# Kernel optimization log

Hardware: AMD Instinct MI355X
Metric: run time of the kernel (lower is better)

Reference implementation:

```python
import jax, jax.numpy as jnp
import numpy as np

N = 100000
E = 1600000
IN_DIM, H1, H2, C = 256, 128, 128, 32


def setup_inputs() -> dict:
    key = jax.random.key(0)
    ks = jax.random.split(key, 8)
    X = jax.random.normal(ks[0], (N, IN_DIM), dtype=jnp.float32)
    edge_index = jax.random.randint(ks[1], (2, E), 0, N, dtype=jnp.int64)
    def glorot(k, shape):
        fan_in, fan_out = shape[0], shape[1]
        lim = (6.0 / (fan_in + fan_out)) ** 0.5
        return jax.random.uniform(k, shape, jnp.float32, -lim, lim)
    W1 = glorot(ks[2], (IN_DIM, H1))
    b1 = jnp.zeros((H1,), jnp.float32)
    W2 = glorot(ks[3], (H1, H2))
    b2 = jnp.zeros((H2,), jnp.float32)
    Wc = glorot(ks[4], (H2, C))
    bc = jnp.zeros((C,), jnp.float32)
    return {"X": X, "edge_index": edge_index, "W1": W1, "b1": b1,
            "W2": W2, "b2": b2, "Wc": Wc, "bc": bc}


def gcn_conv(x, src, dst, dinv, W, b, n):
    # PyG GCNConv: transform, then sym-normalized scatter-add with self-loops
    x = x @ W  # [N, out]
    norm = dinv[src] * dinv[dst]  # [E+N]
    msgs = x[src] * norm[:, None]  # [E+N, out] gather along edges
    out = jax.ops.segment_sum(msgs, dst, num_segments=n)
    return out + b


def reference(X, edge_index, W1, b1, W2, b2, Wc, bc):
    n = X.shape[0]
    loop = jnp.arange(n, dtype=edge_index.dtype)
    src = jnp.concatenate([edge_index[0], loop])
    dst = jnp.concatenate([edge_index[1], loop])
    # degree (with self-loops) at destination nodes
    deg = jax.ops.segment_sum(jnp.ones_like(dst, jnp.float32), dst, num_segments=n)
    dinv = jnp.where(deg > 0, jax.lax.rsqrt(deg), 0.0)
    h = jax.nn.relu(gcn_conv(X, src, dst, dinv, W1, b1, n))
    h = jax.nn.relu(gcn_conv(h, src, dst, dinv, W2, b2, n))
    logits = h @ Wc + bc
    return logits
```

## Files before the change

kernel.cpp:

```cpp
#include <hip/hip_runtime.h>
#include <hip/hip_bf16.h>
#include <hip/hip_fp16.h>

#define IN_DIM 256
#define HDIM 128
#define CDIM 32
#define NSUB 512
#define CHUNK 1024

typedef __attribute__((ext_vector_type(8))) unsigned short u16x8;
typedef __attribute__((ext_vector_type(8))) _Float16 f16x8;
typedef __attribute__((ext_vector_type(4))) float f32x4;
typedef __attribute__((ext_vector_type(4))) int int4v;

__device__ __forceinline__ int swz4(int r) { return (r & 3) ^ ((r >> 2) & 3); }


__global__ void zero512_kernel(int* __restrict__ p) {
    p[blockIdx.x * 256 + threadIdx.x] = 0;
}

__global__ __launch_bounds__(256) void hist512_kernel(const int* __restrict__ dst,
                                                      int* __restrict__ cnt512, int e, int nsr) {
    __shared__ int h[NSUB];
    for (int j = threadIdx.x; j < NSUB; j += 256) h[j] = 0;
    __syncthreads();
    const int stride = gridDim.x * 256;
    for (int i = blockIdx.x * 256 + threadIdx.x; i < e; i += stride) {
        int d = __builtin_nontemporal_load(&dst[i]);
        atomicAdd(&h[(unsigned)d / (unsigned)nsr], 1);
    }
    __syncthreads();
    for (int j = threadIdx.x; j < NSUB; j += 256)
        if (h[j]) atomicAdd(&cnt512[j], h[j]);
}

__global__ __launch_bounds__(256) void scan512_kernel(const int* __restrict__ cnt512,
                                                      int* __restrict__ rp512,
                                                      int* __restrict__ rcur512,
                                                      int* __restrict__ rcur8, int e) {
    __shared__ int sd[256];
    int t = threadIdx.x;
    int v0 = cnt512[2 * t], v1 = cnt512[2 * t + 1];
    sd[t] = v0 + v1;
    __syncthreads();
    for (int off = 1; off < 256; off <<= 1) {
        int x = (t >= off) ? sd[t - off] : 0;
        __syncthreads();
        sd[t] += x;
        __syncthreads();
    }
    int excl = sd[t] - (v0 + v1);
    rp512[2 * t] = excl;       rcur512[2 * t] = excl;
    rp512[2 * t + 1] = excl + v0; rcur512[2 * t + 1] = excl + v0;
    if (t == 255) rp512[512] = e;
    __syncthreads();
    if (t < 8) rcur8[t] = rp512[t * 64];
}

__global__ __launch_bounds__(256) void part8_kernel(
        const int* __restrict__ src, const int* __restrict__ dst,
        int* __restrict__ rcur8, long long* __restrict__ parts8, int e, int nsr) {
    __shared__ int cnt[8], base[8], cnt2[8];
    const int t = threadIdx.x;
    const int nchunk = (e + CHUNK - 1) / CHUNK;
    for (int c = blockIdx.x; c < nchunk; c += gridDim.x) {
        const int b0 = c * CHUNK;
        int s[4], d[4], r[4];
        if (t < 8) { cnt[t] = 0; cnt2[t] = 0; }
        __syncthreads();
        if (b0 + CHUNK <= e) {
            int4v sv = __builtin_nontemporal_load((const int4v*)(src + b0) + t);
            int4v dv = __builtin_nontemporal_load((const int4v*)(dst + b0) + t);
            s[0] = sv.x; s[1] = sv.y; s[2] = sv.z; s[3] = sv.w;
            d[0] = dv.x; d[1] = dv.y; d[2] = dv.z; d[3] = dv.w;
#pragma unroll
            for (int j = 0; j < 4; ++j) {
                r[j] = (int)((unsigned)d[j] / (unsigned)nsr) >> 6;
                atomicAdd(&cnt[r[j]], 1);
            }
        } else {
#pragma unroll
            for (int j = 0; j < 4; ++j) {
                int i = b0 + t * 4 + j;
                if (i < e) {
                    s[j] = src[i]; d[j] = dst[i];
                    r[j] = (int)((unsigned)d[j] / (unsigned)nsr) >> 6;
                    atomicAdd(&cnt[r[j]], 1);
                } else r[j] = -1;
            }
        }
        __syncthreads();
        if (t < 8) base[t] = cnt[t] ? atomicAdd(&rcur8[t], cnt[t]) : 0;
        __syncthreads();
#pragma unroll
        for (int j = 0; j < 4; ++j) {
            if (r[j] >= 0) {
                int off = atomicAdd(&cnt2[r[j]], 1);
                long long v = ((long long)(unsigned)d[j] << 32) | (unsigned)s[j];
                parts8[base[r[j]] + off] = v;
            }
        }
        __syncthreads();
    }
}

__global__ __launch_bounds__(256) void part64_kernel(
        const long long* __restrict__ parts8, const int* __restrict__ rp512,
        int* __restrict__ rcur512, long long* __restrict__ parts, int nsr) {
    __shared__ int cnt[64], base[64], cnt2[64];
    const int t = threadIdx.x;
    const int grp = blockIdx.x & 7;
    const int i0 = rp512[grp * 64];
    const int iE = rp512[grp * 64 + 64];
    const int nbg = gridDim.x >> 3;
    const int bi = blockIdx.x >> 3;
    const int nch = (iE - i0 + CHUNK - 1) / CHUNK;
    for (int c = bi; c < nch; c += nbg) {
        const int b0 = i0 + c * CHUNK;
        long long vv[4]; int r[4];
        if (t < 64) { cnt[t] = 0; cnt2[t] = 0; }
        __syncthreads();
#pragma unroll
        for (int j = 0; j < 4; ++j) {
            int i = b0 + t * 4 + j;
            if (i < iE) {
                vv[j] = parts8[i];
                int d = (int)(vv[j] >> 32);
                r[j] = (int)((unsigned)d / (unsigned)nsr) - grp * 64;
                atomicAdd(&cnt[r[j]], 1);
            } else r[j] = -1;
        }
        __syncthreads();
        if (t < 64) base[t] = cnt[t] ? atomicAdd(&rcur512[grp * 64 + t], cnt[t]) : 0;
        __syncthreads();
#pragma unroll
        for (int j = 0; j < 4; ++j) {
            if (r[j] >= 0) {
                int off = atomicAdd(&cnt2[r[j]], 1);
                parts[base[r[j]] + off] = vv[j];
            }
        }
        __syncthreads();
    }
}

__global__ __launch_bounds__(256) void sortplace_kernel(
        const long long* __restrict__ parts, const int* __restrict__ rp512,
        int* __restrict__ row_ptr, int* __restrict__ csr_src, float* __restrict__ dinv,
        int n, int nsr) {
    __shared__ int hist[256], sd[256], cur[256];
    const int b = blockIdx.x;
    const int d0 = b * nsr;
    if (d0 > n) return;
    const int i0 = rp512[b], iE = rp512[b + 1];
    const int t = threadIdx.x;
    hist[t] = 0;
    __syncthreads();
    for (int i = i0 + t; i < iE; i += 256) {
        int d = (int)(parts[i] >> 32);
        atomicAdd(&hist[d - d0], 1);
    }
    __syncthreads();
    int v = hist[t];
    sd[t] = v;
    __syncthreads();
    for (int off = 1; off < 256; off <<= 1) {
        int x = (t >= off) ? sd[t - off] : 0;
        __syncthreads();
        sd[t] += x;
        __syncthreads();
    }
    int excl = sd[t] - v;
    int node = d0 + t;
    if (t <= nsr && node <= n) row_ptr[node] = i0 + excl;
    if (t < nsr && node < n) dinv[node] = rsqrtf((float)(v + 1));
    cur[t] = i0 + excl;
    __syncthreads();
    for (int i = i0 + t; i < iE; i += 256) {
        long long vv = parts[i];
        int d = (int)(vv >> 32);
        int pos = atomicAdd(&cur[d - d0], 1);
        csr_src[pos] = (int)(vv & 0xffffffffLL);
    }
}


__global__ void wconv_all_kernel(const float* __restrict__ W1, const float* __restrict__ W2,
                                 const float* __restrict__ Wc,
                                 unsigned short* __restrict__ w1t, unsigned short* __restrict__ w2t,
                                 unsigned short* __restrict__ wct) {
    int i = blockIdx.x * 256 + threadIdx.x;
    const int s1 = IN_DIM * HDIM;
    const int s2 = s1 + HDIM * HDIM;
    const int s3 = s2 + HDIM * CDIM;
    if (i < s1) {
        int k = i / HDIM, n2 = i % HDIM;
        w1t[n2 * IN_DIM + k] = __half_as_ushort(__float2half_rn(W1[i]));
    } else if (i < s2) {
        int j = i - s1; int k = j / HDIM, n2 = j % HDIM;
        w2t[n2 * HDIM + k] = __half_as_ushort(__float2half_rn(W2[j]));
    } else if (i < s3) {
        int j = i - s2; int k = j / CDIM, n2 = j % CDIM;
        wct[n2 * HDIM + k] = __half_as_ushort(__float2half_rn(Wc[j]));
    }
}


template<int BN, bool AF16, bool BIAS, bool OUTH>
__global__ __launch_bounds__(256) void gemm_f16_kernel(
        const void* __restrict__ Ap, const unsigned short* __restrict__ Wt,
        const float* __restrict__ bias, void* __restrict__ C, int M, int K) {
    constexpr int FM = 4;
    constexpr int FN = BN / 2 / 16;
    constexpr int BU = (BN * 4 + 255) / 256;
    __shared__ __align__(16) unsigned short As[2][128 * 32];
    __shared__ __align__(16) unsigned short Bs[2][BN * 32];

    const int t = threadIdx.x;
    const int rowBase = blockIdx.x * 128;
    const int l = t & 63, w = t >> 6;
    const int wr = w >> 1, wc = w & 1;
    const int lrow = l & 15, g = l >> 4;
    const int NK = K >> 5;

    f32x4 acc[FM][FN];
#pragma unroll
    for (int i = 0; i < FM; ++i)
#pragma unroll
        for (int j = 0; j < FN; ++j) acc[i][j] = f32x4{0.f, 0.f, 0.f, 0.f};

    u16x8 aS[2];
    float4 af[2][2];
    u16x8 bS[BU];

    auto LOADA = [&](int k0) {
#pragma unroll
        for (int i = 0; i < 2; ++i) {
            int u = t + 256 * i;
            int r = u >> 2, c = u & 3;
            int gr = rowBase + r; if (gr > M - 1) gr = M - 1;
            if (AF16) {
                aS[i] = ((const u16x8*)((const unsigned short*)Ap + (size_t)gr * K + k0))[c];
            } else {
                const float4* ar = (const float4*)((const float*)Ap + (size_t)gr * K + k0);
                af[i][0] = ar[c * 2];
                af[i][1] = ar[c * 2 + 1];
            }
        }
    };
    auto WRITEA = [&](int buf) {
#pragma unroll
        for (int i = 0; i < 2; ++i) {
            int u = t + 256 * i;
            int r = u >> 2, c = u & 3;
            int d = r * 4 + (c ^ swz4(r));
            if (AF16) {
                ((u16x8*)As[buf])[d] = aS[i];
            } else {
                f16x8 h;
                h[0] = (_Float16)af[i][0].x; h[1] = (_Float16)af[i][0].y;
                h[2] = (_Float16)af[i][0].z; h[3] = (_Float16)af[i][0].w;
                h[4] = (_Float16)af[i][1].x; h[5] = (_Float16)af[i][1].y;
                h[6] = (_Float16)af[i][1].z; h[7] = (_Float16)af[i][1].w;
                ((f16x8*)As[buf])[d] = h;
            }
        }
    };
    auto LOADB = [&](int k0) {
#pragma unroll
        for (int i = 0; i < BU; ++i) {
            int u = t + 256 * i;
            if (u < BN * 4) {
                int nn = u >> 2, c = u & 3;
                bS[i] = ((const u16x8*)(Wt + (size_t)nn * K + k0))[c];
            }
        }
    };
    auto WRITEB = [&](int buf) {
#pragma unroll
        for (int i = 0; i < BU; ++i) {
            int u = t + 256 * i;
            if (u < BN * 4) {
                int nn = u >> 2, c = u & 3;
                ((u16x8*)Bs[buf])[nn * 4 + (c ^ swz4(nn))] = bS[i];
            }
        }
    };

    LOADA(0); LOADB(0);
    WRITEA(0); WRITEB(0);
    __syncthreads();

    for (int k = 0; k < NK; ++k) {
        int cur = k & 1;
        bool more = (k + 1 < NK);
        if (more) { LOADA((k + 1) << 5); LOADB((k + 1) << 5); }

        f16x8 a[FM], b[FN];
#pragma unroll
        for (int fm = 0; fm < FM; ++fm) {
            int r = wr * 64 + fm * 16 + lrow;
            a[fm] = ((const f16x8*)As[cur])[r * 4 + (g ^ swz4(r))];
        }
#pragma unroll
        for (int fn = 0; fn < FN; ++fn) {
            int nn = wc * (FN * 16) + fn * 16 + lrow;
            b[fn] = ((const f16x8*)Bs[cur])[nn * 4 + (g ^ swz4(nn))];
        }
#pragma unroll
        for (int fm = 0; fm < FM; ++fm)
#pragma unroll
            for (int fn = 0; fn < FN; ++fn)
                acc[fm][fn] = __builtin_amdgcn_mfma_f32_16x16x32_f16(a[fm], b[fn], acc[fm][fn], 0, 0, 0);

        if (more) { WRITEA(cur ^ 1); WRITEB(cur ^ 1); }
        __syncthreads();
    }

#pragma unroll
    for (int fm = 0; fm < FM; ++fm)
#pragma unroll
        for (int fn = 0; fn < FN; ++fn) {
            int col = wc * (FN * 16) + fn * 16 + lrow;
#pragma unroll
            for (int r = 0; r < 4; ++r) {
                int row = rowBase + wr * 64 + fm * 16 + g * 4 + r;
                if (row < M) {
                    float v = acc[fm][fn][r];
                    if (BIAS) v += bias[col];
                    if (OUTH) ((__half*)C)[(size_t)row * BN + col] = __float2half_rn(v);
                    else      ((float*)C)[(size_t)row * BN + col] = v;
                }
            }
        }
}


__global__ __launch_bounds__(256) void gather_kernel(
        const __half* __restrict__ x, const int* __restrict__ row_ptr,
        const int* __restrict__ csr_src, const float* __restrict__ dinv,
        const float* __restrict__ bias, __half* __restrict__ out, int n) {
    int node = __builtin_amdgcn_readfirstlane(blockIdx.x * 4 + (threadIdx.x >> 6));
    if (node >= n) return;
    int lane = threadIdx.x & 63;
    const __half2* xv = (const __half2*)x;
    float dd = dinv[node];
    float2 self = __half22float2(xv[(size_t)node * 64 + lane]);
    float accx = dd * self.x, accy = dd * self.y;
    int p = row_ptr[node], end = row_ptr[node + 1];
    for (; p + 7 < end; p += 8) {
        int s[8]; float w[8]; float2 v[8];
#pragma unroll
        for (int j = 0; j < 8; ++j) s[j] = csr_src[p + j];
#pragma unroll
        for (int j = 0; j < 8; ++j) w[j] = dinv[s[j]];
#pragma unroll
        for (int j = 0; j < 8; ++j) v[j] = __half22float2(xv[(size_t)s[j] * 64 + lane]);
#pragma unroll
        for (int j = 0; j < 8; ++j) { accx += w[j] * v[j].x; accy += w[j] * v[j].y; }
    }
    for (; p + 3 < end; p += 4) {
        int s0 = csr_src[p], s1 = csr_src[p + 1], s2 = csr_src[p + 2], s3 = csr_src[p + 3];
        float w0 = dinv[s0], w1 = dinv[s1], w2 = dinv[s2], w3 = dinv[s3];
        float2 v0 = __half22float2(xv[(size_t)s0 * 64 + lane]);
        float2 v1 = __half22float2(xv[(size_t)s1 * 64 + lane]);
        float2 v2 = __half22float2(xv[(size_t)s2 * 64 + lane]);
        float2 v3 = __half22float2(xv[(size_t)s3 * 64 + lane]);
        accx += w0 * v0.x + w1 * v1.x + w2 * v2.x + w3 * v3.x;
        accy += w0 * v0.y + w1 * v1.y + w2 * v2.y + w3 * v3.y;
    }
    for (; p < end; ++p) {
        int s0 = csr_src[p];
        float w0 = dinv[s0];
        float2 v0 = __half22float2(xv[(size_t)s0 * 64 + lane]);
        accx += w0 * v0.x;
        accy += w0 * v0.y;
    }
    float2 bb = ((const float2*)bias)[lane];
    float2 r;
    r.x = fmaxf(accx * dd + bb.x, 0.f);
    r.y = fmaxf(accy * dd + bb.y, 0.f);
    ((__half2*)out)[(size_t)node * 64 + lane] = __float22half2_rn(r);
}


__global__ __launch_bounds__(256) void gather_cls_kernel(
        const __half* __restrict__ x, const int* __restrict__ row_ptr,
        const int* __restrict__ csr_src, const float* __restrict__ dinv,
        const float* __restrict__ b2, const unsigned short* __restrict__ wct,
        const float* __restrict__ bc, float* __restrict__ out, int n) {
    __shared__ __align__(16) __half h_lds[16][136];
    const int w = threadIdx.x >> 6;
    const int lane = threadIdx.x & 63;
    const int node0 = blockIdx.x * 16;
    const __half2* xv = (const __half2*)x;
    const float2 bb = ((const float2*)b2)[lane];

#pragma unroll
    for (int j = 0; j < 4; ++j) {
        int row = w * 4 + j;
        int node = __builtin_amdgcn_readfirstlane(node0 + row);
        float2 rv = make_float2(0.f, 0.f);
        if (node < n) {
            float dd = dinv[node];
            float2 self = __half22float2(xv[(size_t)node * 64 + lane]);
            float accx = dd * self.x, accy = dd * self.y;
            int p = row_ptr[node], end = row_ptr[node + 1];
            for (; p + 7 < end; p += 8) {
                int s[8]; float wt[8]; float2 v[8];
#pragma unroll
                for (int q = 0; q < 8; ++q) s[q] = csr_src[p + q];
#pragma unroll
                for (int q = 0; q < 8; ++q) wt[q] = dinv[s[q]];
#pragma unroll
                for (int q = 0; q < 8; ++q) v[q] = __half22float2(xv[(size_t)s[q] * 64 + lane]);
#pragma unroll
                for (int q = 0; q < 8; ++q) { accx += wt[q] * v[q].x; accy += wt[q] * v[q].y; }
            }
            for (; p + 3 < end; p += 4) {
                int s0 = csr_src[p], s1 = csr_src[p + 1], s2 = csr_src[p + 2], s3 = csr_src[p + 3];
                float w0 = dinv[s0], w1 = dinv[s1], w2 = dinv[s2], w3 = dinv[s3];
                float2 v0 = __half22float2(xv[(size_t)s0 * 64 + lane]);
                float2 v1 = __half22float2(xv[(size_t)s1 * 64 + lane]);
                float2 v2 = __half22float2(xv[(size_t)s2 * 64 + lane]);
                float2 v3 = __half22float2(xv[(size_t)s3 * 64 + lane]);
                accx += w0 * v0.x + w1 * v1.x + w2 * v2.x + w3 * v3.x;
                accy += w0 * v0.y + w1 * v1.y + w2 * v2.y + w3 * v3.y;
            }
            for (; p < end; ++p) {
                int s0 = csr_src[p];
                float w0 = dinv[s0];
                float2 v0 = __half22float2(xv[(size_t)s0 * 64 + lane]);
                accx += w0 * v0.x;
                accy += w0 * v0.y;
            }
            rv.x = fmaxf(accx * dd + bb.x, 0.f);
            rv.y = fmaxf(accy * dd + bb.y, 0.f);
        }
        *(__half2*)&h_lds[row][2 * lane] = __float22half2_rn(rv);
    }
    __syncthreads();

    if (w == 0) {
        const int lrow = lane & 15, g = lane >> 4;
        f32x4 acc[2];
        acc[0] = f32x4{0.f, 0.f, 0.f, 0.f};
        acc[1] = f32x4{0.f, 0.f, 0.f, 0.f};
#pragma unroll
        for (int k0 = 0; k0 < HDIM; k0 += 32) {
            f16x8 a = *(const f16x8*)&h_lds[lrow][k0 + 8 * g];
#pragma unroll
            for (int fn = 0; fn < 2; ++fn) {
                f16x8 b = *(const f16x8*)((const _Float16*)wct + (fn * 16 + lrow) * HDIM + k0 + 8 * g);
                acc[fn] = __builtin_amdgcn_mfma_f32_16x16x32_f16(a, b, acc[fn], 0, 0, 0);
            }
        }
#pragma unroll
        for (int fn = 0; fn < 2; ++fn) {
            int col = fn * 16 + lrow;
            float bcv = bc[col];
#pragma unroll
            for (int r = 0; r < 4; ++r) {
                int node = node0 + g * 4 + r;
                if (node < n) out[(size_t)node * CDIM + col] = acc[fn][r] + bcv;
            }
        }
    }
}


extern "C" void kernel_launch(void* const* d_in, const int* in_sizes, int n_in,
                              void* d_out, int out_size, void* d_ws, size_t ws_size,
                              hipStream_t stream) {
    const float* X  = (const float*)d_in[0];
    const int*   ei = (const int*)d_in[1];
    const float* W1 = (const float*)d_in[2];
    const float* b1 = (const float*)d_in[3];
    const float* W2 = (const float*)d_in[4];
    const float* b2 = (const float*)d_in[5];
    const float* Wc = (const float*)d_in[6];
    const float* bc = (const float*)d_in[7];
    float* out = (float*)d_out;

    const int n = in_sizes[0] / IN_DIM;
    const int e = in_sizes[1] / 2;
    const int* src = ei;
    const int* dst = ei + e;
    const int nsr = (n + NSUB - 1) / NSUB;

    char* ws = (char*)d_ws;
    auto align = [](size_t x) { return (x + 255) & ~(size_t)255; };
    size_t off = 0;
    float* dinv   = (float*)(ws + off); off += align((size_t)n * 4);
    int* row_ptr  = (int*)(ws + off);   off += align((size_t)(n + 1) * 4);
    int* cnt512   = (int*)(ws + off);   off += align(512 * 4);
    int* rp512    = (int*)(ws + off);   off += align(513 * 4);
    int* rcur512  = (int*)(ws + off);   off += align(512 * 4);
    int* rcur8    = (int*)(ws + off);   off += align(8 * 4);
    long long* parts8 = (long long*)(ws + off); off += align((size_t)e * 8);
    long long* parts  = (long long*)(ws + off); off += align((size_t)e * 8);
    unsigned short* w1t = (unsigned short*)(ws + off); off += align((size_t)IN_DIM * HDIM * 2);
    unsigned short* w2t = (unsigned short*)(ws + off); off += align((size_t)HDIM * HDIM * 2);
    unsigned short* wct = (unsigned short*)(ws + off); off += align((size_t)HDIM * CDIM * 2);
    __half* bufAh = (__half*)(ws + off); off += align((size_t)n * HDIM * 2);
    __half* bufBh = (__half*)(ws + off); off += align((size_t)n * HDIM * 2);
    int* csr_src  = (int*)parts8;

    wconv_all_kernel<<<(IN_DIM * HDIM + HDIM * HDIM + HDIM * CDIM + 255) / 256, 256, 0, stream>>>(
        W1, W2, Wc, w1t, w2t, wct);

    zero512_kernel<<<2, 256, 0, stream>>>(cnt512);
    hist512_kernel<<<256, 256, 0, stream>>>(dst, cnt512, e, nsr);
    scan512_kernel<<<1, 256, 0, stream>>>(cnt512, rp512, rcur512, rcur8, e);
    part8_kernel<<<1024, 256, 0, stream>>>(src, dst, rcur8, parts8, e, nsr);
    part64_kernel<<<1024, 256, 0, stream>>>(parts8, rp512, rcur512, parts, nsr);
    sortplace_kernel<<<NSUB, 256, 0, stream>>>(parts, rp512, row_ptr, csr_src, dinv, n, nsr);

    const int gBlocks = (n + 127) / 128;
    const int nb_g = (n + 3) / 4;

    gemm_f16_kernel<128, false, false, true><<<gBlocks, 256, 0, stream>>>(X, w1t, nullptr, bufAh, n, IN_DIM);
    gather_kernel<<<nb_g, 256, 0, stream>>>(bufAh, row_ptr, csr_src, dinv, b1, bufBh, n);

    gemm_f16_kernel<128, true, false, true><<<gBlocks, 256, 0, stream>>>(bufBh, w2t, nullptr, bufAh, n, HDIM);

    gather_cls_kernel<<<(n + 15) / 16, 256, 0, stream>>>(bufAh, row_ptr, csr_src, dinv, b2, wct, bc, out, n);
}
```

Before: 254.9 us.

## Replace two-pass radix partition with single LDS-staged 512-bucket partition

Merges the 8-way then 64-way partition passes into one kernel that bins each 4096-edge chunk into 512 buckets, scans local counts, stages the packed edges in LDS in bucket order and writes them out in coalesced runs. This removes one full read and write of the 8-byte edge array and the intermediate buffer, but adds a per-chunk block scan and 512 global atomics per chunk. It also switches the half-precision outputs of the GEMM and gather kernels to nontemporal stores, and gives csr_src its own buffer instead of aliasing the removed one.

```diff
diff --git a/kernel.cpp b/kernel.cpp
--- a/kernel.cpp
+++ b/kernel.cpp
@@ -6,7 +6,7 @@
 #define HDIM 128
 #define CDIM 32
 #define NSUB 512
-#define CHUNK 1024
+#define PCHUNK 4096
 
 typedef __attribute__((ext_vector_type(8))) unsigned short u16x8;
 typedef __attribute__((ext_vector_type(8))) _Float16 f16x8;
@@ -37,8 +37,7 @@
 
 __global__ __launch_bounds__(256) void scan512_kernel(const int* __restrict__ cnt512,
                                                       int* __restrict__ rp512,
-                                                      int* __restrict__ rcur512,
-                                                      int* __restrict__ rcur8, int e) {
+                                                      int* __restrict__ rcur512, int e) {
     __shared__ int sd[256];
     int t = threadIdx.x;
     int v0 = cnt512[2 * t], v1 = cnt512[2 * t + 1];
@@ -51,95 +50,79 @@
         __syncthreads();
     }
     int excl = sd[t] - (v0 + v1);
-    rp512[2 * t] = excl;       rcur512[2 * t] = excl;
+    rp512[2 * t] = excl;          rcur512[2 * t] = excl;
     rp512[2 * t + 1] = excl + v0; rcur512[2 * t + 1] = excl + v0;
     if (t == 255) rp512[512] = e;
-    __syncthreads();
-    if (t < 8) rcur8[t] = rp512[t * 64];
-}
-
-__global__ __launch_bounds__(256) void part8_kernel(
+}
+
+__global__ __launch_bounds__(256) void part512_kernel(
         const int* __restrict__ src, const int* __restrict__ dst,
-        int* __restrict__ rcur8, long long* __restrict__ parts8, int e, int nsr) {
-    __shared__ int cnt[8], base[8], cnt2[8];
+        int* __restrict__ rcur512, long long* __restrict__ parts, int e, int nsr) {
+    __shared__ long long staged[PCHUNK];
+    __shared__ int hist[NSUB], lbase[NSUB], gbase[NSUB], lcur[NSUB];
+    __shared__ int sd[256];
     const int t = threadIdx.x;
-    const int nchunk = (e + CHUNK - 1) / CHUNK;
-    for (int c = blockIdx.x; c < nchunk; c += gridDim.x) {
-        const int b0 = c * CHUNK;
-        int s[4], d[4], r[4];
-        if (t < 8) { cnt[t] = 0; cnt2[t] = 0; }
-        __syncthreads();
-        if (b0 + CHUNK <= e) {
-            int4v sv = __builtin_nontemporal_load((const int4v*)(src + b0) + t);
-            int4v dv = __builtin_nontemporal_load((const int4v*)(dst + b0) + t);
-            s[0] = sv.x; s[1] = sv.y; s[2] = sv.z; s[3] = sv.w;
-            d[0] = dv.x; d[1] = dv.y; d[2] = dv.z; d[3] = dv.w;
-#pragma unroll
-            for (int j = 0; j < 4; ++j) {
-                r[j] = (int)((unsigned)d[j] / (unsigned)nsr) >> 6;
-                atomicAdd(&cnt[r[j]], 1);
+    const int nch = (e + PCHUNK - 1) / PCHUNK;
+    for (int c = blockIdx.x; c < nch; c += gridDim.x) {
+        const int b0 = c * PCHUNK;
+        const int cnt = (b0 + PCHUNK <= e) ? PCHUNK : (e - b0);
+        int s[16], d[16], bn[16];
+        hist[2 * t] = 0; hist[2 * t + 1] = 0;
+        __syncthreads();
+        if (cnt == PCHUNK) {
+#pragma unroll
+            for (int q = 0; q < 4; ++q) {
+                int u = q * 256 + t;
+                int4v sv = __builtin_nontemporal_load((const int4v*)(src + b0) + u);
+                int4v dv = __builtin_nontemporal_load((const int4v*)(dst + b0) + u);
+                s[4 * q] = sv.x; s[4 * q + 1] = sv.y; s[4 * q + 2] = sv.z; s[4 * q + 3] = sv.w;
+                d[4 * q] = dv.x; d[4 * q + 1] = dv.y; d[4 * q + 2] = dv.z; d[4 * q + 3] = dv.w;
+            }
+#pragma unroll
+            for (int j = 0; j < 16; ++j) {
+                bn[j] = (int)((unsigned)d[j] / (unsigned)nsr);
+                atomicAdd(&hist[bn[j]], 1);
             }
         } else {
 #pragma unroll
-            for (int j = 0; j < 4; ++j) {
-                int i = b0 + t * 4 + j;
-                if (i < e) {
+            for (int j = 0; j < 16; ++j) {
+                int u = (j / 4) * 1024 + t * 4 + (j & 3);
+                int i = b0 + u;
+                if (u < cnt) {
                     s[j] = src[i]; d[j] = dst[i];
-                    r[j] = (int)((unsigned)d[j] / (unsigned)nsr) >> 6;
-                    atomicAdd(&cnt[r[j]], 1);
-                } else r[j] = -1;
-            }
-        }
-        __syncthreads();
-        if (t < 8) base[t] = cnt[t] ? atomicAdd(&rcur8[t], cnt[t]) : 0;
-        __syncthreads();
-#pragma unroll
-        for (int j = 0; j < 4; ++j) {
-            if (r[j] >= 0) {
-                int off = atomicAdd(&cnt2[r[j]], 1);
-                long long v = ((long long)(unsigned)d[j] << 32) | (unsigned)s[j];
-                parts8[base[r[j]] + off] = v;
-            }
-        }
-        __syncthreads();
-    }
-}
-
-__global__ __launch_bounds__(256) void part64_kernel(
-        const long long* __restrict__ parts8, const int* __restrict__ rp512,
-        int* __restrict__ rcur512, long long* __restrict__ parts, int nsr) {
-    __shared__ int cnt[64], base[64], cnt2[64];
-    const int t = threadIdx.x;
-    const int grp = blockIdx.x & 7;
-    const int i0 = rp512[grp * 64];
-    const int iE = rp512[grp * 64 + 64];
-    const int nbg = gridDim.x >> 3;
-    const int bi = blockIdx.x >> 3;
-    const int nch = (iE - i0 + CHUNK - 1) / CHUNK;
-    for (int c = bi; c < nch; c += nbg) {
-        const int b0 = i0 + c * CHUNK;
-        long long vv[4]; int r[4];
-        if (t < 64) { cnt[t] = 0; cnt2[t] = 0; }
-        __syncthreads();
-#pragma unroll
-        for (int j = 0; j < 4; ++j) {
-            int i = b0 + t * 4 + j;
-            if (i < iE) {
-                vv[j] = parts8[i];
-                int d = (int)(vv[j] >> 32);
-                r[j] = (int)((unsigned)d / (unsigned)nsr) - grp * 64;
-                atomicAdd(&cnt[r[j]], 1);
-            } else r[j] = -1;
-        }
-        __syncthreads();
-        if (t < 64) base[t] = cnt[t] ? atomicAdd(&rcur512[grp * 64 + t], cnt[t]) : 0;
-        __syncthreads();
-#pragma unroll
-        for (int j = 0; j < 4; ++j) {
-            if (r[j] >= 0) {
-                int off = atomicAdd(&cnt2[r[j]], 1);
-                parts[base[r[j]] + off] = vv[j];
-            }
+                    bn[j] = (int)((unsigned)d[j] / (unsigned)nsr);
+                    atomicAdd(&hist[bn[j]], 1);
+                } else bn[j] = -1;
+            }
+        }
+        __syncthreads();
+        int h0 = hist[2 * t], h1 = hist[2 * t + 1];
+        sd[t] = h0 + h1;
+        __syncthreads();
+        for (int off = 1; off < 256; off <<= 1) {
+            int x = (t >= off) ? sd[t - off] : 0;
+            __syncthreads();
+            sd[t] += x;
+            __syncthreads();
+        }
+        int excl = sd[t] - (h0 + h1);
+        lbase[2 * t] = excl;          lcur[2 * t] = excl;
+        lbase[2 * t + 1] = excl + h0; lcur[2 * t + 1] = excl + h0;
+        gbase[2 * t]     = h0 ? atomicAdd(&rcur512[2 * t], h0) : 0;
+        gbase[2 * t + 1] = h1 ? atomicAdd(&rcur512[2 * t + 1], h1) : 0;
+        __syncthreads();
+#pragma unroll
+        for (int j = 0; j < 16; ++j) {
+            if (bn[j] >= 0) {
+                int pos = atomicAdd(&lcur[bn[j]], 1);
+                staged[pos] = ((long long)(unsigned)d[j] << 32) | (unsigned)s[j];
+            }
+        }
+        __syncthreads();
+        for (int i = t; i < cnt; i += 256) {
+            long long v = staged[i];
+            int b = (int)((unsigned)(int)(v >> 32) / (unsigned)nsr);
+            parts[gbase[b] + (i - lbase[b])] = v;
         }
         __syncthreads();
     }
@@ -329,8 +312,13 @@
                 if (row < M) {
                     float v = acc[fm][fn][r];
                     if (BIAS) v += bias[col];
-                    if (OUTH) ((__half*)C)[(size_t)row * BN + col] = __float2half_rn(v);
-                    else      ((float*)C)[(size_t)row * BN + col] = v;
+                    if (OUTH) {
+                        __builtin_nontemporal_store(
+                            __half_as_ushort(__float2half_rn(v)),
+                            (unsigned short*)C + (size_t)row * BN + col);
+                    } else {
+                        ((float*)C)[(size_t)row * BN + col] = v;
+                    }
                 }
             }
         }
@@ -381,7 +369,9 @@
     float2 r;
     r.x = fmaxf(accx * dd + bb.x, 0.f);
     r.y = fmaxf(accy * dd + bb.y, 0.f);
-    ((__half2*)out)[(size_t)node * 64 + lane] = __float22half2_rn(r);
+    __half2 hv = __float22half2_rn(r);
+    __builtin_nontemporal_store(*(unsigned int*)&hv,
+                                (unsigned int*)((__half2*)out + (size_t)node * 64 + lane));
 }
 
 
@@ -497,24 +487,21 @@
     int* cnt512   = (int*)(ws + off);   off += align(512 * 4);
     int* rp512    = (int*)(ws + off);   off += align(513 * 4);
     int* rcur512  = (int*)(ws + off);   off += align(512 * 4);
-    int* rcur8    = (int*)(ws + off);   off += align(8 * 4);
-    long long* parts8 = (long long*)(ws + off); off += align((size_t)e * 8);
-    long long* parts  = (long long*)(ws + off); off += align((size_t)e * 8);
+    long long* parts = (long long*)(ws + off); off += align((size_t)e * 8);
+    int* csr_src  = (int*)(ws + off);   off += align((size_t)e * 4);
     unsigned short* w1t = (unsigned short*)(ws + off); off += align((size_t)IN_DIM * HDIM * 2);
     unsigned short* w2t = (unsigned short*)(ws + off); off += align((size_t)HDIM * HDIM * 2);
     unsigned short* wct = (unsigned short*)(ws + off); off += align((size_t)HDIM * CDIM * 2);
     __half* bufAh = (__half*)(ws + off); off += align((size_t)n * HDIM * 2);
     __half* bufBh = (__half*)(ws + off); off += align((size_t)n * HDIM * 2);
-    int* csr_src  = (int*)parts8;
 
     wconv_all_kernel<<<(IN_DIM * HDIM + HDIM * HDIM + HDIM * CDIM + 255) / 256, 256, 0, stream>>>(
         W1, W2, Wc, w1t, w2t, wct);
 
     zero512_kernel<<<2, 256, 0, stream>>>(cnt512);
     hist512_kernel<<<256, 256, 0, stream>>>(dst, cnt512, e, nsr);
-    scan512_kernel<<<1, 256, 0, stream>>>(cnt512, rp512, rcur512, rcur8, e);
-    part8_kernel<<<1024, 256, 0, stream>>>(src, dst, rcur8, parts8, e, nsr);
-    part64_kernel<<<1024, 256, 0, stream>>>(parts8, rp512, rcur512, parts, nsr);
+    scan512_kernel<<<1, 256, 0, stream>>>(cnt512, rp512, rcur512, e);
+    part512_kernel<<<512, 256, 0, stream>>>(src, dst, rcur512, parts, e, nsr);
     sortplace_kernel<<<NSUB, 256, 0, stream>>>(parts, rp512, row_ptr, csr_src, dinv, n, nsr);
 
     const int gBlocks = (n + 127) / 128;
```

Result: faster. 249.2 us, median of 2 (-2.2%).
